# Optimization experiments

Hardware: AMD Instinct MI355X
Metric: run time of the kernel (lower is better)

## Reference

```python
import jax, jax.numpy as jnp
import numpy as np

EPS = 1e-12


def l2_normalize(x, axis=-1, eps=EPS):
    return x * jax.lax.rsqrt((x * x).sum(axis=axis, keepdims=True) + eps)


def setup_inputs() -> dict:
    key = jax.random.key(0)
    k1, k2 = jax.random.split(key)
    B, S, E_DIM = 32, 1024, 32   # batch, tokens per image, codebook embed dim
    N_EMBED = 8192               # codebook size
    hidden_states = jax.random.normal(k1, (B, S, E_DIM), dtype=jnp.float32)
    # variance_scaling(1.0, 'fan_in', 'normal') over fan_in=E_DIM -> std = 1/sqrt(E_DIM)
    embedding = jax.random.normal(k2, (N_EMBED, E_DIM), dtype=jnp.float32) / jnp.sqrt(jnp.float32(E_DIM))
    return {"hidden_states": hidden_states, "embedding": embedding}


def reference(hidden_states, embedding):
    e_dim = embedding.shape[-1]
    # flatten to (N, e_dim) and L2-normalize both codes and inputs
    flat = l2_normalize(hidden_states.reshape(-1, e_dim), axis=1)   # (N, e_dim)
    emb = l2_normalize(embedding, axis=1)                           # (K, e_dim)
    # pairwise squared L2 distance: ||z||^2 + ||e||^2 - 2 z.e  -> (N, K)
    distance = (
        jnp.sum(flat * flat, axis=1, keepdims=True)
        + jnp.sum(emb * emb, axis=1)
        - 2.0 * jnp.dot(flat, emb.T)
    )
    min_encoding_indices = jnp.argmin(distance, axis=1).reshape(hidden_states.shape[0], -1)  # (B, S)
    # codebook lookup (gather raw embedding then renormalize, as in get_codebook_entry)
    z_q = l2_normalize(jnp.take(embedding, min_encoding_indices, axis=0), axis=-1)  # (B, S, e_dim)
    hidden_states_normed = l2_normalize(hidden_states, axis=-1)
    e_latent_loss = jnp.mean(jnp.square(jax.lax.stop_gradient(z_q) - hidden_states_normed))
    q_latent_loss = jnp.mean(jnp.square(z_q - jax.lax.stop_gradient(hidden_states_normed)))
    # straight-through estimator
    z_q = hidden_states + jax.lax.stop_gradient(z_q - hidden_states)
    return (z_q, min_encoding_indices, q_latent_loss, e_latent_loss)
```

## Files before the change

### kernel.cpp

```cpp
#include <hip/hip_runtime.h>
#include <math.h>

#define N_TOK   32768
#define K_CODES 8192
#define E_DIM   32
#define BLK     256
#define NCHUNK  8
#define TPC     64
#define TT      4
#define TAU     2e-4f
#define RG      4

#define OUT_IDX  1048576
#define OUT_QL   1081344
#define OUT_EL   1081345

#define WSB_BPK    0
#define WSB_PBEST  1052672
#define WSB_PSEC   2101248
#define WSB_PIDX   3149824
#define WSB_FIDX   3674112
#define WSB_FCNT   3805184
#define WSB_FLIST  3805312
#define WSB_LPART  3936384

typedef __attribute__((ext_vector_type(8))) short bf16x8;
typedef __attribute__((ext_vector_type(4))) float f32x4;
typedef __attribute__((ext_vector_type(4))) double f64x4;

__device__ inline unsigned short bf16_rne(float x) {
  unsigned u = __builtin_bit_cast(unsigned, x);
  unsigned r = u + 0x7FFFu + ((u >> 16) & 1u);
  return (unsigned short)(r >> 16);
}
__device__ inline float bf16_to_f32(unsigned short h) {
  return __builtin_bit_cast(float, (unsigned)h << 16);
}

__global__ __launch_bounds__(BLK) void prep_emb_kernel(
    const float* __restrict__ emb, char* __restrict__ Bpk)
{
  const int c = blockIdx.x * BLK + threadIdx.x;
  float z[E_DIM];
  const float4* p = (const float4*)(emb + c * E_DIM);
  float s = 0.f;
#pragma unroll
  for (int q = 0; q < 8; ++q) {
    float4 v = p[q];
    ((float4*)z)[q] = v;
    s += v.x * v.x + v.y * v.y + v.z * v.z + v.w * v.w;
  }
  const float rn = 1.f / sqrtf(s + 1e-12f);
  const int tile = c >> 4, row = c & 15;
#pragma unroll
  for (int g = 0; g < 4; ++g) {
    bf16x8 h8, l8;
#pragma unroll
    for (int j = 0; j < 8; ++j) {
      const float zn = z[g * 8 + j] * rn;
      const unsigned short h = bf16_rne(zn);
      h8[j] = (short)h;
      l8[j] = (short)bf16_rne(zn - bf16_to_f32(h));
    }
    char* base = Bpk + (size_t)tile * 2048 + (size_t)(g * 16 + row) * 16;
    *(bf16x8*)(base) = h8;
    *(bf16x8*)(base + 1024) = l8;
  }
}

__global__ __launch_bounds__(256) void prep64_kernel(
    const float* __restrict__ emb, double* __restrict__ rza,
    double* __restrict__ nsqa)
{
  const int c = blockIdx.x * 256 + threadIdx.x;
  const float4* p = (const float4*)(emb + c * E_DIM);
  float4 v[8];
  double n2 = 0.0;
#pragma unroll
  for (int q = 0; q < 8; ++q) {
    v[q] = p[q];
    const double ex = v[q].x, ey = v[q].y, ez = v[q].z, ew = v[q].w;
    n2 = fma(ew, ew, fma(ez, ez, fma(ey, ey, fma(ex, ex, n2))));
  }
  const double rz = 1.0 / sqrt(n2 + 1e-12);
  double nsq = 0.0;
#pragma unroll
  for (int q = 0; q < 8; ++q) {
    const double ex = (double)v[q].x * rz, ey = (double)v[q].y * rz;
    const double ez = (double)v[q].z * rz, ew = (double)v[q].w * rz;
    nsq = fma(ew, ew, fma(ez, ez, fma(ey, ey, fma(ex, ex, nsq))));
  }
  rza[c] = rz;
  nsqa[c] = nsq;
}

__global__ __launch_bounds__(BLK, 4) void screen_kernel(
    const float* __restrict__ hs, const char* __restrict__ Bpk,
    float* __restrict__ pbest, float* __restrict__ psec,
    unsigned short* __restrict__ pidx)
{
  const int lane = threadIdx.x & 63;
  const int wave = threadIdx.x >> 6;
  const int grp = lane >> 4, row = lane & 15;
  const int chunk = blockIdx.x >> 7;
  const int tb = blockIdx.x & 127;
  const int tile0 = tb * 16 + wave * TT;

  bf16x8 ahi[TT], alo[TT];
#pragma unroll
  for (int tt = 0; tt < TT; ++tt) {
    const float* ap = hs + ((tile0 + tt) * 16 + row) * E_DIM + grp * 8;
    float a[8];
    ((float4*)a)[0] = ((const float4*)ap)[0];
    ((float4*)a)[1] = ((const float4*)ap)[1];
    float ps = 0.f;
#pragma unroll
    for (int j = 0; j < 8; ++j) ps = fmaf(a[j], a[j], ps);
    ps += __shfl_xor(ps, 16, 64);
    ps += __shfl_xor(ps, 32, 64);
    const float rn = 1.f / sqrtf(ps + 1e-12f);
#pragma unroll
    for (int j = 0; j < 8; ++j) {
      const float zn = a[j] * rn;
      const unsigned short h = bf16_rne(zn);
      ahi[tt][j] = (short)h;
      alo[tt][j] = (short)bf16_rne(zn - bf16_to_f32(h));
    }
  }

  float best[TT][4], sec[TT][4];
  int bct[TT][4];
#pragma unroll
  for (int tt = 0; tt < TT; ++tt)
#pragma unroll
    for (int r = 0; r < 4; ++r) { best[tt][r] = -3e38f; sec[tt][r] = -3e38f; bct[tt][r] = 0; }

  const f32x4 Z4 = {0.f, 0.f, 0.f, 0.f};
  const char* Bc = Bpk + (size_t)(chunk * TPC) * 2048 + (size_t)lane * 16;

#define PROC(CH, CL, CTV)                                                      \
  {                                                                            \
    f32x4 acc[TT];                                                             \
    _Pragma("unroll") for (int tt = 0; tt < TT; ++tt) {                        \
      acc[tt] = __builtin_amdgcn_mfma_f32_16x16x32_bf16(ahi[tt], (CH), Z4, 0, 0, 0); \
      acc[tt] = __builtin_amdgcn_mfma_f32_16x16x32_bf16(ahi[tt], (CL), acc[tt], 0, 0, 0); \
      acc[tt] = __builtin_amdgcn_mfma_f32_16x16x32_bf16(alo[tt], (CH), acc[tt], 0, 0, 0); \
    }                                                                          \
    _Pragma("unroll") for (int tt = 0; tt < TT; ++tt)                          \
    _Pragma("unroll") for (int r = 0; r < 4; ++r) {                            \
      const float d = acc[tt][r];                                              \
      sec[tt][r] = __builtin_amdgcn_fmed3f(best[tt][r], sec[tt][r], d);        \
      if (d > best[tt][r]) { best[tt][r] = d; bct[tt][r] = (CTV); }            \
    }                                                                          \
  }

  bf16x8 h0 = *(const bf16x8*)(Bc);
  bf16x8 l0 = *(const bf16x8*)(Bc + 1024);
  bf16x8 h1 = *(const bf16x8*)(Bc + 2048);
  bf16x8 l1 = *(const bf16x8*)(Bc + 3072);
  for (int ct = 0; ct < TPC; ct += 2) {
    const bf16x8 ch0 = h0, cl0 = l0, ch1 = h1, cl1 = l1;
    const char* pn = Bc + (size_t)(ct + 2) * 2048;
    h0 = *(const bf16x8*)(pn);
    l0 = *(const bf16x8*)(pn + 1024);
    h1 = *(const bf16x8*)(pn + 2048);
    l1 = *(const bf16x8*)(pn + 3072);
    PROC(ch0, cl0, ct)
    PROC(ch1, cl1, ct + 1)
  }
#undef PROC

  const int base = chunk * N_TOK;
#pragma unroll
  for (int tt = 0; tt < TT; ++tt) {
#pragma unroll
    for (int r = 0; r < 4; ++r) {
      float b = best[tt][r], s = sec[tt][r];
      int id = bct[tt][r] * 16 + row;
#pragma unroll
      for (int w = 1; w < 16; w <<= 1) {
        const float ob = __shfl_xor(b, w, 64);
        const float os = __shfl_xor(s, w, 64);
        const int   oi = __shfl_xor(id, w, 64);
        s = fmaxf(fmaxf(s, os), fminf(b, ob));
        if (ob > b || (ob == b && oi < id)) id = oi;
        b = fmaxf(b, ob);
      }
      if (row == 0) {
        const int tok = (tile0 + tt) * 16 + grp * 4 + r;
        pbest[base + tok] = b;
        psec[base + tok] = s;
        pidx[base + tok] = (unsigned short)(chunk * 1024 + id);
      }
    }
  }
}

__global__ __launch_bounds__(BLK) void merge_kernel(
    const float* __restrict__ pbest, const float* __restrict__ psec,
    const unsigned short* __restrict__ pidx, int* __restrict__ fidx,
    int* __restrict__ flagcnt, int* __restrict__ flaglist)
{
  const int t = blockIdx.x * BLK + threadIdx.x;
  float best = -3e38f, sec = -3e38f;
  int code = 0;
#pragma unroll
  for (int ch = 0; ch < NCHUNK; ++ch) {
    const float b = pbest[ch * N_TOK + t];
    const float s = psec[ch * N_TOK + t];
    const int c = pidx[ch * N_TOK + t];
    if (b > best) { sec = fmaxf(best, s); best = b; code = c; }
    else          { sec = fmaxf(sec, b); }
  }
  fidx[t] = code;
  if (best - sec < TAU) {
    const int p = atomicAdd(flagcnt, 1);
    flaglist[p] = t;
  }
}

__global__ __launch_bounds__(256, 1) void recheck_kernel(
    const float* __restrict__ hs, const float* __restrict__ emb,
    const double* __restrict__ rza, const double* __restrict__ nsqa,
    const int* __restrict__ flagcnt, const int* __restrict__ flaglist,
    int* __restrict__ fidx)
{
  __shared__ __align__(16) double zsh[RG][E_DIM];
  __shared__ int tsh[RG];
  __shared__ double rvW[RG][4];
  __shared__ int riW[RG][4];
  const int tid = threadIdx.x;
  const int lane = tid & 63, wv = tid >> 6;
  const int nflag = *flagcnt;
  for (int base = blockIdx.x * RG; base < nflag; base += gridDim.x * RG) {
    __syncthreads();
    if (tid < 128) {
      const int g = tid >> 5, j = tid & 31;
      const bool act = (base + g) < nflag;
      const int t = act ? flaglist[base + g] : -1;
      if (j == 0) tsh[g] = t;
      const double zj = act ? (double)hs[t * E_DIM + j] : 0.0;
      double sq = zj * zj;
#pragma unroll
      for (int o = 16; o > 0; o >>= 1) sq += __shfl_xor(sq, o, 32);
      const double rzt = 1.0 / sqrt(sq + 1e-12);
      zsh[g][j] = zj * rzt;
    }
    __syncthreads();

    double bobj[RG];
    int bidx[RG];
#pragma unroll
    for (int g = 0; g < RG; ++g) { bobj[g] = 1e300; bidx[g] = 0x7fffffff; }

    for (int c = tid; c < K_CODES; c += 256) {
      const float4* ep = (const float4*)(emb + c * E_DIM);
      f64x4 e64[8];
#pragma unroll
      for (int q = 0; q < 8; ++q) {
        const float4 v = ep[q];
        e64[q][0] = (double)v.x; e64[q][1] = (double)v.y;
        e64[q][2] = (double)v.z; e64[q][3] = (double)v.w;
      }
      const double rzc = rza[c], nsqc = nsqa[c];
#pragma unroll
      for (int g = 0; g < RG; ++g) {
        double d0 = 0.0, d1 = 0.0;
#pragma unroll
        for (int q = 0; q < 8; q += 2) {
#pragma unroll
          for (int x = 0; x < 4; ++x) {
            d0 = fma(e64[q][x],     zsh[g][q * 4 + x],       d0);
            d1 = fma(e64[q + 1][x], zsh[g][(q + 1) * 4 + x], d1);
          }
        }
        const double obj = fma(-2.0, (d0 + d1) * rzc, nsqc);
        if (obj < bobj[g]) { bobj[g] = obj; bidx[g] = c; }
      }
    }

#pragma unroll
    for (int g = 0; g < RG; ++g) {
      double b = bobj[g]; int i = bidx[g];
#pragma unroll
      for (int o = 32; o > 0; o >>= 1) {
        const double ob = __shfl_down(b, o, 64);
        const int oi = __shfl_down(i, o, 64);
        if (ob < b || (ob == b && oi < i)) { b = ob; i = oi; }
      }
      if (lane == 0) { rvW[g][wv] = b; riW[g][wv] = i; }
    }
    __syncthreads();
    if (tid < RG) {
      const int g = tid;
      double b = rvW[g][0]; int i = riW[g][0];
#pragma unroll
      for (int w = 1; w < 4; ++w) {
        const double ob = rvW[g][w]; const int oi = riW[g][w];
        if (ob < b || (ob == b && oi < i)) { b = ob; i = oi; }
      }
      const int t = tsh[g];
      if (t >= 0) fidx[t] = i;
    }
  }
}

__global__ __launch_bounds__(BLK) void finalize_kernel(
    const float* __restrict__ hs, const float* __restrict__ emb,
    const int* __restrict__ fidx, float* __restrict__ out,
    float* __restrict__ lpart)
{
  const int t = blockIdx.x * BLK + threadIdx.x;
  const int idx = fidx[t];
  const float4* ep = (const float4*)(emb + idx * E_DIM);
  const float4* hp = (const float4*)(hs + t * E_DIM);
  float4 e[8], h[8];
  float se = 0.f, sh = 0.f;
#pragma unroll
  for (int q = 0; q < 8; ++q) {
    e[q] = ep[q]; h[q] = hp[q];
    se += e[q].x * e[q].x + e[q].y * e[q].y + e[q].z * e[q].z + e[q].w * e[q].w;
    sh += h[q].x * h[q].x + h[q].y * h[q].y + h[q].z * h[q].z + h[q].w * h[q].w;
  }
  const float re = 1.f / sqrtf(se + 1e-12f);
  const float rh = 1.f / sqrtf(sh + 1e-12f);
  float4* zo = (float4*)(out + t * E_DIM);
  float err = 0.f;
#pragma unroll
  for (int q = 0; q < 8; ++q) {
    float4 zq, hn;
    zq.x = e[q].x * re; zq.y = e[q].y * re; zq.z = e[q].z * re; zq.w = e[q].w * re;
    hn.x = h[q].x * rh; hn.y = h[q].y * rh; hn.z = h[q].z * rh; hn.w = h[q].w * rh;
    float dx = zq.x - hn.x, dy = zq.y - hn.y, dz = zq.z - hn.z, dw = zq.w - hn.w;
    err += dx * dx + dy * dy + dz * dz + dw * dw;
    zo[q] = zq;
  }
  out[OUT_IDX + t] = (float)idx;
#pragma unroll
  for (int o = 32; o > 0; o >>= 1) err += __shfl_down(err, o);
  if ((threadIdx.x & 63) == 0) lpart[t >> 6] = err;
}

__global__ __launch_bounds__(256) void loss_kernel(
    const float* __restrict__ lpart, float* __restrict__ out)
{
  const int tid = threadIdx.x;
  float a = lpart[tid] + lpart[tid + 256];
#pragma unroll
  for (int o = 32; o > 0; o >>= 1) a += __shfl_down(a, o);
  __shared__ float w[4];
  if ((tid & 63) == 0) w[tid >> 6] = a;
  __syncthreads();
  if (tid == 0) {
    const float tot = (w[0] + w[1]) + (w[2] + w[3]);
    const float c = tot * (1.0f / 1048576.0f);
    out[OUT_QL] = c;
    out[OUT_EL] = c;
  }
}

extern "C" void kernel_launch(void* const* d_in, const int* in_sizes, int n_in,
                              void* d_out, int out_size, void* d_ws, size_t ws_size,
                              hipStream_t stream) {
  (void)in_sizes; (void)n_in; (void)out_size; (void)ws_size;
  const float* hs  = (const float*)d_in[0];
  const float* emb = (const float*)d_in[1];
  float* out = (float*)d_out;
  char* wsb = (char*)d_ws;

  char*           Bpk    = wsb + WSB_BPK;
  float*          pbest  = (float*)(wsb + WSB_PBEST);
  float*          psec   = (float*)(wsb + WSB_PSEC);
  unsigned short* pidx   = (unsigned short*)(wsb + WSB_PIDX);
  int*            fidx   = (int*)(wsb + WSB_FIDX);
  int*            flagcnt= (int*)(wsb + WSB_FCNT);
  int*            flist  = (int*)(wsb + WSB_FLIST);
  float*          lpart  = (float*)(wsb + WSB_LPART);
  double*         rza    = (double*)(wsb + WSB_PBEST);
  double*         nsqa   = (double*)(wsb + WSB_PBEST + 65536);

  hipMemsetAsync(flagcnt, 0, sizeof(int), stream);

  prep_emb_kernel<<<dim3(K_CODES / BLK), BLK, 0, stream>>>(emb, Bpk);
  screen_kernel<<<dim3(NCHUNK * 128), BLK, 0, stream>>>(hs, Bpk, pbest, psec, pidx);
  merge_kernel<<<dim3(N_TOK / BLK), BLK, 0, stream>>>(pbest, psec, pidx, fidx, flagcnt, flist);
  prep64_kernel<<<dim3(K_CODES / 256), 256, 0, stream>>>(emb, rza, nsqa);
  recheck_kernel<<<dim3(512), 256, 0, stream>>>(hs, emb, rza, nsqa, flagcnt, flist, fidx);
  finalize_kernel<<<dim3(N_TOK / BLK), BLK, 0, stream>>>(hs, emb, fidx, out, lpart);
  loss_kernel<<<dim3(1), 256, 0, stream>>>(lpart, out);
}
```

Baseline: 136.0 us.

## Split codebook into 16 chunks and build flag list via scan instead of atomics

Doubles the number of codebook chunks in the screening pass (halving codes per block) to raise parallelism, storing the extra partial results in scratch space within the output buffer. Replaces the atomic-append flag list and its memset with a flags array, a per-block ballot count, a single-block prefix scan and a scatter kernel, which gives a deterministic ordering. This adds two kernel launches and doubles the partial-result traffic in the merge step. It also relies on the output buffer regions being overwritten later by finalize.

```diff
diff --git a/kernel.cpp b/kernel.cpp
--- a/kernel.cpp
+++ b/kernel.cpp
@@ -5,8 +5,8 @@
 #define K_CODES 8192
 #define E_DIM   32
 #define BLK     256
-#define NCHUNK  8
-#define TPC     64
+#define NCHUNK  16
+#define TPC     32
 #define TT      4
 #define TAU     2e-4f
 #define RG      4
@@ -14,15 +14,21 @@
 #define OUT_IDX  1048576
 #define OUT_QL   1081344
 #define OUT_EL   1081345
+#define OUTS_PB2   0
+#define OUTS_PS2   262144
+#define OUTS_PI2   524288
+#define OUTS_FLAGS 655360
+#define OUTS_FLIST 688128
+#define OUTS_BCNT  720896
+#define OUTS_BOFF  721024
+#define OUTS_NFLAG 721152
 
 #define WSB_BPK    0
 #define WSB_PBEST  1052672
 #define WSB_PSEC   2101248
 #define WSB_PIDX   3149824
 #define WSB_FIDX   3674112
-#define WSB_FCNT   3805184
-#define WSB_FLIST  3805312
-#define WSB_LPART  3936384
+#define WSB_LPART  3805184
 
 typedef __attribute__((ext_vector_type(8))) short bf16x8;
 typedef __attribute__((ext_vector_type(4))) float f32x4;
@@ -96,8 +102,8 @@
 
 __global__ __launch_bounds__(BLK, 4) void screen_kernel(
     const float* __restrict__ hs, const char* __restrict__ Bpk,
-    float* __restrict__ pbest, float* __restrict__ psec,
-    unsigned short* __restrict__ pidx)
+    float* __restrict__ pb1, float* __restrict__ ps1, unsigned short* __restrict__ pi1,
+    float* __restrict__ pb2, float* __restrict__ ps2, unsigned short* __restrict__ pi2)
 {
   const int lane = threadIdx.x & 63;
   const int wave = threadIdx.x >> 6;
@@ -170,7 +176,10 @@
   }
 #undef PROC
 
-  const int base = chunk * N_TOK;
+  float* __restrict__ pbest = (chunk < 8) ? pb1 : pb2;
+  float* __restrict__ psec  = (chunk < 8) ? ps1 : ps2;
+  unsigned short* __restrict__ pidx = (chunk < 8) ? pi1 : pi2;
+  const int base = (chunk & 7) * N_TOK;
 #pragma unroll
   for (int tt = 0; tt < TT; ++tt) {
 #pragma unroll
@@ -190,39 +199,92 @@
         const int tok = (tile0 + tt) * 16 + grp * 4 + r;
         pbest[base + tok] = b;
         psec[base + tok] = s;
-        pidx[base + tok] = (unsigned short)(chunk * 1024 + id);
+        pidx[base + tok] = (unsigned short)(chunk * 512 + id);
       }
     }
   }
 }
 
 __global__ __launch_bounds__(BLK) void merge_kernel(
-    const float* __restrict__ pbest, const float* __restrict__ psec,
-    const unsigned short* __restrict__ pidx, int* __restrict__ fidx,
-    int* __restrict__ flagcnt, int* __restrict__ flaglist)
+    const float* __restrict__ pb1, const float* __restrict__ ps1,
+    const unsigned short* __restrict__ pi1,
+    const float* __restrict__ pb2, const float* __restrict__ ps2,
+    const unsigned short* __restrict__ pi2,
+    int* __restrict__ fidx, unsigned* __restrict__ flags,
+    int* __restrict__ bcount)
 {
   const int t = blockIdx.x * BLK + threadIdx.x;
   float best = -3e38f, sec = -3e38f;
   int code = 0;
 #pragma unroll
   for (int ch = 0; ch < NCHUNK; ++ch) {
-    const float b = pbest[ch * N_TOK + t];
-    const float s = psec[ch * N_TOK + t];
-    const int c = pidx[ch * N_TOK + t];
+    const int o = (ch & 7) * N_TOK + t;
+    const float b = (ch < 8) ? pb1[o] : pb2[o];
+    const float s = (ch < 8) ? ps1[o] : ps2[o];
+    const int c = (ch < 8) ? pi1[o] : pi2[o];
     if (b > best) { sec = fmaxf(best, s); best = b; code = c; }
     else          { sec = fmaxf(sec, b); }
   }
   fidx[t] = code;
-  if (best - sec < TAU) {
-    const int p = atomicAdd(flagcnt, 1);
-    flaglist[p] = t;
+  const unsigned f = (best - sec < TAU) ? 1u : 0u;
+  flags[t] = f;
+  __shared__ int wcnt[4];
+  const unsigned long long m = __ballot(f != 0);
+  if ((threadIdx.x & 63) == 0) wcnt[threadIdx.x >> 6] = (int)__popcll(m);
+  __syncthreads();
+  if (threadIdx.x == 0)
+    bcount[blockIdx.x] = wcnt[0] + wcnt[1] + wcnt[2] + wcnt[3];
+}
+
+__global__ __launch_bounds__(128) void scan_kernel(
+    const int* __restrict__ bcount, int* __restrict__ boff,
+    int* __restrict__ nflagp)
+{
+  __shared__ int sh[128];
+  const int tid = threadIdx.x;
+  const int c = bcount[tid];
+  sh[tid] = c;
+  __syncthreads();
+#pragma unroll
+  for (int off = 1; off < 128; off <<= 1) {
+    int v = 0;
+    if (tid >= off) v = sh[tid - off];
+    __syncthreads();
+    sh[tid] += v;
+    __syncthreads();
+  }
+  boff[tid] = sh[tid] - c;
+  if (tid == 127) *nflagp = sh[127];
+}
+
+__global__ __launch_bounds__(BLK) void scatter_kernel(
+    const unsigned* __restrict__ flags, const int* __restrict__ boff,
+    int* __restrict__ flaglist)
+{
+  const int tid = threadIdx.x;
+  const int t = blockIdx.x * BLK + tid;
+  const unsigned f = flags[t];
+  const int lane = tid & 63, wv = tid >> 6;
+  const unsigned long long m = __ballot(f != 0);
+  __shared__ int wtot[4], woff[4];
+  if (lane == 0) wtot[wv] = (int)__popcll(m);
+  __syncthreads();
+  if (tid == 0) {
+    int s = 0;
+#pragma unroll
+    for (int w = 0; w < 4; ++w) { woff[w] = s; s += wtot[w]; }
+  }
+  __syncthreads();
+  if (f) {
+    const int rank = (int)__popcll(m & ((1ull << lane) - 1ull));
+    flaglist[boff[blockIdx.x] + woff[wv] + rank] = t;
   }
 }
 
 __global__ __launch_bounds__(256, 1) void recheck_kernel(
     const float* __restrict__ hs, const float* __restrict__ emb,
     const double* __restrict__ rza, const double* __restrict__ nsqa,
-    const int* __restrict__ flagcnt, const int* __restrict__ flaglist,
+    const int* __restrict__ nflagp, const int* __restrict__ flaglist,
     int* __restrict__ fidx)
 {
   __shared__ __align__(16) double zsh[RG][E_DIM];
@@ -231,7 +293,7 @@
   __shared__ int riW[RG][4];
   const int tid = threadIdx.x;
   const int lane = tid & 63, wv = tid >> 6;
-  const int nflag = *flagcnt;
+  const int nflag = *nflagp;
   for (int base = blockIdx.x * RG; base < nflag; base += gridDim.x * RG) {
     __syncthreads();
     if (tid < 128) {
@@ -368,24 +430,30 @@
   float* out = (float*)d_out;
   char* wsb = (char*)d_ws;
 
-  char*           Bpk    = wsb + WSB_BPK;
-  float*          pbest  = (float*)(wsb + WSB_PBEST);
-  float*          psec   = (float*)(wsb + WSB_PSEC);
-  unsigned short* pidx   = (unsigned short*)(wsb + WSB_PIDX);
-  int*            fidx   = (int*)(wsb + WSB_FIDX);
-  int*            flagcnt= (int*)(wsb + WSB_FCNT);
-  int*            flist  = (int*)(wsb + WSB_FLIST);
-  float*          lpart  = (float*)(wsb + WSB_LPART);
-  double*         rza    = (double*)(wsb + WSB_PBEST);
-  double*         nsqa   = (double*)(wsb + WSB_PBEST + 65536);
-
-  hipMemsetAsync(flagcnt, 0, sizeof(int), stream);
+  char*           Bpk   = wsb + WSB_BPK;
+  float*          pb1   = (float*)(wsb + WSB_PBEST);
+  float*          ps1   = (float*)(wsb + WSB_PSEC);
+  unsigned short* pi1   = (unsigned short*)(wsb + WSB_PIDX);
+  int*            fidx  = (int*)(wsb + WSB_FIDX);
+  float*          lpart = (float*)(wsb + WSB_LPART);
+  double*         rza   = (double*)(wsb + WSB_PBEST);
+  double*         nsqa  = (double*)(wsb + WSB_PBEST + 65536);
+  float*          pb2     = out + OUTS_PB2;
+  float*          ps2     = out + OUTS_PS2;
+  unsigned short* pi2     = (unsigned short*)(out + OUTS_PI2);
+  unsigned*       flags   = (unsigned*)(out + OUTS_FLAGS);
+  int*            flist   = (int*)(out + OUTS_FLIST);
+  int*            bcount  = (int*)(out + OUTS_BCNT);
+  int*            boff    = (int*)(out + OUTS_BOFF);
+  int*            nflagp  = (int*)(out + OUTS_NFLAG);
 
   prep_emb_kernel<<<dim3(K_CODES / BLK), BLK, 0, stream>>>(emb, Bpk);
-  screen_kernel<<<dim3(NCHUNK * 128), BLK, 0, stream>>>(hs, Bpk, pbest, psec, pidx);
-  merge_kernel<<<dim3(N_TOK / BLK), BLK, 0, stream>>>(pbest, psec, pidx, fidx, flagcnt, flist);
+  screen_kernel<<<dim3(NCHUNK * 128), BLK, 0, stream>>>(hs, Bpk, pb1, ps1, pi1, pb2, ps2, pi2);
+  merge_kernel<<<dim3(N_TOK / BLK), BLK, 0, stream>>>(pb1, ps1, pi1, pb2, ps2, pi2, fidx, flags, bcount);
+  scan_kernel<<<dim3(1), 128, 0, stream>>>(bcount, boff, nflagp);
+  scatter_kernel<<<dim3(N_TOK / BLK), BLK, 0, stream>>>(flags, boff, flist);
   prep64_kernel<<<dim3(K_CODES / 256), 256, 0, stream>>>(emb, rza, nsqa);
-  recheck_kernel<<<dim3(512), 256, 0, stream>>>(hs, emb, rza, nsqa, flagcnt, flist, fidx);
+  recheck_kernel<<<dim3(512), 256, 0, stream>>>(hs, emb, rza, nsqa, nflagp, flist, fidx);
   finalize_kernel<<<dim3(N_TOK / BLK), BLK, 0, stream>>>(hs, emb, fidx, out, lpart);
   loss_kernel<<<dim3(1), 256, 0, stream>>>(lpart, out);
 }
```

Result: slower. 144.9 us (+6.5%).
